# Kernel tuning notes

Measured on AMD Instinct MI355X. Metric: run time of the kernel, lower is better.

The kernel has to match this reference:

```python
import jax, jax.numpy as jnp
import numpy as np

SCALE = 1.0 / np.sqrt(512.0).astype(np.float32)  # attention() hardcodes d_k=512


def setup_inputs() -> dict:
    key = jax.random.key(0)
    ks = jax.random.split(key, 9)
    B, S, D = 4, 2048, 512
    mk = lambda k, shape: jax.random.normal(k, shape, dtype=jnp.float32) * 0.05
    return {
        "q": mk(ks[0], (B, S, D)),
        "k": mk(ks[1], (B, S, D)),
        "v": mk(ks[2], (B, S, D)),
        "WQ_w": mk(ks[3], (D, D)),
        "WQ_b": mk(ks[4], (D,)),
        "WK_w": mk(ks[5], (D, D)),
        "WK_b": mk(ks[6], (D,)),
        "WV_w": mk(ks[7], (D, D)),
        "WV_b": mk(ks[8], (D,)),
    }


def reference(q, k, v, WQ_w, WQ_b, WK_w, WK_b, WV_w, WV_b):
    # torch nn.Linear: y = x @ W.T + b
    qp = q @ WQ_w.T + WQ_b  # [B,S,dk]
    kp = k @ WK_w.T + WK_b  # [B,S,dk]
    vp = v @ WV_w.T + WV_b  # [B,S,dv]
    qk = jnp.einsum("bqd,bkd->bqk", qp, kp) * SCALE  # [B,Sq,Sk]
    S = qk.shape[1]
    tril = jnp.tril(jnp.ones((S, S), dtype=qk.dtype))  # multiplicative causal mask
    qk = qk * tril
    # NOTE: original applies softmax over dim=1 (the query axis), faithfully kept.
    attn = jax.nn.softmax(qk, axis=1)
    out = jnp.einsum("bqk,bkd->bqd", attn, vp)  # [B,Sq,dv]
    return out
```

## Files before the change

### kernel.cpp

```cpp
#include <hip/hip_runtime.h>
#include <hip/hip_bf16.h>


#define S_LEN 2048
#define D_DIM 512
#define SCALE_F 0.044194173824159216f

typedef __attribute__((ext_vector_type(8))) short s8v;
typedef __attribute__((ext_vector_type(4))) short s4v;
typedef __attribute__((ext_vector_type(4))) float f4v;

enum { EPI_BIAS = 0, EPI_BIAS_T = 1, EPI_SCORES = 2 };

#define SBAR()    asm volatile("s_barrier" ::: "memory")
#define WAITV(n)  asm volatile("s_waitcnt vmcnt(" #n ")" ::: "memory")

__device__ __forceinline__ short f2bf_s(float f) {
  union { __hip_bfloat16 b; short s; } u; u.b = __float2bfloat16(f); return u.s;
}
__device__ __forceinline__ float bf2f_s(short h) {
  union { short s; __hip_bfloat16 b; } u; u.s = h; return __bfloat162float(u.b);
}

__device__ __forceinline__ void glds16(const short* g, short* l) {
  __builtin_amdgcn_global_load_lds((const __attribute__((address_space(1))) void*)g,
                                   (__attribute__((address_space(3))) void*)l, 16, 0, 0);
}

template <int EPI>
__device__ __forceinline__ void gemm_core(
    const short* __restrict__ A, const short* __restrict__ B,
    short* __restrict__ C, const float* __restrict__ bias,
    short* SMEM, int N, int K, size_t sCz, int m0, int n0, int bz,
    float* __restrict__ Z)
{
  const int tid  = threadIdx.x;
  const int w    = tid >> 6;
  const int lane = tid & 63;
  const int quad = lane >> 4;
  const int l16  = lane & 15;
  const int wm   = (w >> 1) * 64;
  const int wn   = (w & 1) * 64;

  const int strow = tid >> 2;
  const int gl = ((tid & 3) ^ (strow & 3)) * 8;

  f4v acc[4][4];
#pragma unroll
  for (int i = 0; i < 4; ++i)
#pragma unroll
    for (int j = 0; j < 4; ++j)
#pragma unroll
      for (int r = 0; r < 4; ++r) acc[i][j][r] = 0.0f;

  const short* Ag = A + (size_t)(m0 + strow) * K + gl;
  const short* Bg = B + (size_t)(n0 + strow) * K + gl;
  const size_t pstr = (size_t)64 * K;
  const int t8 = tid * 8;
  const int swq = l16 & 3;

  const int niter = K >> 5;

#pragma unroll
  for (int t = 0; t < 2; ++t) {
    const int k0 = t << 5;
    short* dst = SMEM + t * 8192 + t8;
#pragma unroll
    for (int p = 0; p < 2; ++p) glds16(Ag + k0 + p * pstr, dst + p * 2048);
#pragma unroll
    for (int p = 0; p < 2; ++p) glds16(Bg + k0 + p * pstr, dst + 4096 + p * 2048);
  }

  int cb = 0;
  for (int i = 0; i < niter; ++i) {
    if (i + 1 < niter) { WAITV(4); } else { WAITV(0); }
    SBAR();

    if (i + 2 < niter) {
      int nb = cb + 2; if (nb >= 3) nb -= 3;
      const int k2 = (i + 2) << 5;
      short* dst = SMEM + nb * 8192 + t8;
#pragma unroll
      for (int p = 0; p < 2; ++p) glds16(Ag + k2 + p * pstr, dst + p * 2048);
#pragma unroll
      for (int p = 0; p < 2; ++p) glds16(Bg + k2 + p * pstr, dst + 4096 + p * 2048);
    }

    const short* As = SMEM + cb * 8192;
    const short* Bs = As + 4096;
    cb = (cb == 2) ? 0 : cb + 1;

    s8v af[4], bf[4];
#pragma unroll
    for (int ii = 0; ii < 4; ++ii)
      af[ii] = *(const s8v*)&As[(wm + ii * 16 + l16) * 32 + ((quad ^ swq) * 8)];
#pragma unroll
    for (int j = 0; j < 4; ++j)
      bf[j] = *(const s8v*)&Bs[(wn + j * 16 + l16) * 32 + ((quad ^ swq) * 8)];
#pragma unroll
    for (int ii = 0; ii < 4; ++ii)
#pragma unroll
      for (int j = 0; j < 4; ++j)
        acc[ii][j] = __builtin_amdgcn_mfma_f32_16x16x32_bf16(af[ii], bf[j], acc[ii][j], 0, 0, 0);
  }

  float bv[4];
  if (EPI == EPI_BIAS || EPI == EPI_BIAS_T) {
#pragma unroll
    for (int j = 0; j < 4; ++j) bv[j] = bias[n0 + wn + j * 16 + l16];
  }

  if (EPI == EPI_BIAS_T) {
#pragma unroll
    for (int i = 0; i < 4; ++i) {
#pragma unroll
      for (int j = 0; j < 4; ++j) {
        const int gn  = n0 + wn + j * 16 + l16;
        const int gmb = m0 + wm + i * 16 + quad * 4;
        const int bb = gmb >> 11, ssb = gmb & (S_LEN - 1);
        s4v o;
#pragma unroll
        for (int r = 0; r < 4; ++r) o[r] = f2bf_s(acc[i][j][r] + bv[j]);
        *(s4v*)&C[((size_t)bb * D_DIM + gn) * S_LEN + ssb] = o;
      }
    }
    return;
  }

  short* TB = SMEM;
  const int wbase = w * 2176;
  float csum[4] = {0.f, 0.f, 0.f, 0.f};

#pragma unroll
  for (int ph = 0; ph < 2; ++ph) {
    __syncthreads();
#pragma unroll
    for (int ii = 0; ii < 2; ++ii) {
      const int i = ph * 2 + ii;
#pragma unroll
      for (int j = 0; j < 4; ++j) {
        const int gn = n0 + wn + j * 16 + l16;
#pragma unroll
        for (int r = 0; r < 4; ++r) {
          short o;
          if (EPI == EPI_SCORES) {
            const int gm = m0 + wm + i * 16 + quad * 4 + r;
            const float f = (gm >= gn) ? (__expf(acc[i][j][r] * SCALE_F) - 1.0f) : 0.0f;
            csum[j] += f;
            o = f2bf_s(f);
          } else {
            o = f2bf_s(acc[i][j][r] + bv[j]);
          }
          TB[wbase + (ii * 16 + quad * 4 + r) * 68 + j * 16 + l16] = o;
        }
      }
    }
    __syncthreads();
#pragma unroll
    for (int p = 0; p < 4; ++p) {
      const int row = p * 8 + (lane >> 3);
      const int cg  = lane & 7;
      const s8v vv = *(const s8v*)&TB[wbase + row * 68 + cg * 8];
      const int gm = m0 + wm + ph * 32 + row;
      const int gn = n0 + wn + cg * 8;
      *(s8v*)&C[sCz + (size_t)gm * N + gn] = vv;
    }
  }

  if (EPI == EPI_SCORES) {
#pragma unroll
    for (int j = 0; j < 4; ++j) {
      float cs = csum[j];
      cs += __shfl_xor(cs, 16, 64);
      cs += __shfl_xor(cs, 32, 64);
      if (quad == 0) atomicAdd(&Z[(bz << 11) + n0 + wn + j * 16 + l16], cs);
    }
  }
}

__global__ __launch_bounds__(256, 3) void gemm_scoresF(
    const short* __restrict__ A, const short* __restrict__ B, short* __restrict__ C,
    float* __restrict__ Z)
{
  __shared__ __align__(16) short SMEM[24576];
  const int bz = blockIdx.z;
  const int t = blockIdx.x;
  int ti = (int)((sqrtf(8.0f * t + 1.0f) - 1.0f) * 0.5f);
  while ((ti + 1) * (ti + 2) / 2 <= t) ++ti;
  while (ti * (ti + 1) / 2 > t) --ti;
  const int tj = t - ti * (ti + 1) / 2;
  gemm_core<EPI_SCORES>(A + (size_t)bz * S_LEN * D_DIM, B + (size_t)bz * S_LEN * D_DIM,
                        C, nullptr, SMEM, S_LEN, D_DIM,
                        (size_t)bz * S_LEN * S_LEN, ti * 128, tj * 128, bz, Z);
}

__global__ __launch_bounds__(256, 3) void proj3(
    const short* __restrict__ a0, const short* __restrict__ a1, const short* __restrict__ a2,
    const short* __restrict__ b0, const short* __restrict__ b1, const short* __restrict__ b2,
    short* __restrict__ c0, short* __restrict__ c1, short* __restrict__ c2,
    const float* __restrict__ x0, const float* __restrict__ x1, const float* __restrict__ x2)
{
  __shared__ __align__(16) short SMEM[24576];
  const int z = blockIdx.z;
  const short* A = (z == 0) ? a0 : (z == 1) ? a1 : a2;
  const short* B = (z == 0) ? b0 : (z == 1) ? b1 : b2;
  short*       C = (z == 0) ? c0 : (z == 1) ? c1 : c2;
  const float* bias = (z == 0) ? x0 : (z == 1) ? x1 : x2;
  if (z == 2)
    gemm_core<EPI_BIAS_T>(A, B, C, bias, SMEM, D_DIM, D_DIM, 0,
                          blockIdx.y * 128, blockIdx.x * 128, 0, nullptr);
  else
    gemm_core<EPI_BIAS>(A, B, C, bias, SMEM, D_DIM, D_DIM, 0,
                        blockIdx.y * 128, blockIdx.x * 128, 0, nullptr);
}

__global__ __launch_bounds__(256, 2) void gemm_outF(
    const short* __restrict__ F, const short* __restrict__ vpT,
    const float* __restrict__ Tv, float* __restrict__ out)
{
  __shared__ __align__(16) short SMEM[36864];

  const int tid  = threadIdx.x;
  const int bz   = blockIdx.y;
  const int zs   = blockIdx.z;
  const int mi   = (zs < 16) ? (31 - zs) : (zs - 16);
  const int m0   = mi * 64;
  const int n0   = blockIdx.x * 128;

  const short* A = F   + (size_t)bz * S_LEN * S_LEN;
  const short* B = vpT + (size_t)bz * D_DIM * S_LEN;

  const int w    = tid >> 6;
  const int lane = tid & 63;
  const int quad = lane >> 4;
  const int l16  = lane & 15;
  const int wm   = (w >> 1) * 32;
  const int wn   = (w & 1) * 64;

  const int strow = tid >> 3;
  const int gl = ((tid & 7) ^ (strow & 7)) * 8;

  f4v acc[2][4];
#pragma unroll
  for (int i = 0; i < 2; ++i)
#pragma unroll
    for (int j = 0; j < 4; ++j)
#pragma unroll
      for (int r = 0; r < 4; ++r) acc[i][j][r] = 0.0f;

  const short* Ag = A + (size_t)(m0 + strow) * S_LEN + gl;
  const short* Bg = B + (size_t)(n0 + strow) * S_LEN + gl;
  const size_t pstr = (size_t)32 * S_LEN;
  const int t8 = tid * 8;
  const int swq = l16 & 7;

  const int niter = (m0 >> 6) + 1;

#pragma unroll
  for (int pre = 0; pre < 2; ++pre) {
    short* dst = SMEM + pre * 12288 + t8;
    const int k0 = pre << 6;
#pragma unroll
    for (int p = 0; p < 2; ++p) glds16(Ag + k0 + p * pstr, dst + p * 2048);
#pragma unroll
    for (int p = 0; p < 4; ++p) glds16(Bg + k0 + p * pstr, dst + 4096 + p * 2048);
  }

  int cbuf = 0;
  for (int i = 0; i < niter; ++i) {
    if (i + 1 < niter) { WAITV(6); } else { WAITV(0); }
    SBAR();

    if (i + 2 < niter) {
      int nb = cbuf + 2; if (nb >= 3) nb -= 3;
      const int k2 = (i + 2) << 6;
      short* dst = SMEM + nb * 12288 + t8;
#pragma unroll
      for (int p = 0; p < 2; ++p) glds16(Ag + k2 + p * pstr, dst + p * 2048);
#pragma unroll
      for (int p = 0; p < 4; ++p) glds16(Bg + k2 + p * pstr, dst + 4096 + p * 2048);
    }

    const short* As = SMEM + cbuf * 12288;
    const short* Bs = As + 4096;
    cbuf = (cbuf == 2) ? 0 : cbuf + 1;
#pragma unroll
    for (int kk = 0; kk < 2; ++kk) {
      s8v af[2], bf[4];
#pragma unroll
      for (int ii = 0; ii < 2; ++ii)
        af[ii] = *(const s8v*)&As[(wm + ii * 16 + l16) * 64 + (((kk * 4 + quad) ^ swq) * 8)];
#pragma unroll
      for (int j = 0; j < 4; ++j)
        bf[j] = *(const s8v*)&Bs[(wn + j * 16 + l16) * 64 + (((kk * 4 + quad) ^ swq) * 8)];
#pragma unroll
      for (int ii = 0; ii < 2; ++ii)
#pragma unroll
        for (int j = 0; j < 4; ++j)
          acc[ii][j] = __builtin_amdgcn_mfma_f32_16x16x32_bf16(af[ii], bf[j], acc[ii][j], 0, 0, 0);
    }
  }

  float* Cf = out + (size_t)bz * S_LEN * D_DIM;
#pragma unroll
  for (int i = 0; i < 2; ++i) {
#pragma unroll
    for (int j = 0; j < 4; ++j) {
      const int gn = n0 + wn + j * 16 + l16;
      const float tvn = Tv[(bz << 9) + gn];
#pragma unroll
      for (int r = 0; r < 4; ++r) {
        const int gm = m0 + wm + i * 16 + quad * 4 + r;
        Cf[(size_t)gm * D_DIM + gn] = acc[i][j][r] + tvn;
      }
    }
  }
}

__global__ __launch_bounds__(256) void cvt3(
    const float* __restrict__ s0, const float* __restrict__ s1,
    const float* __restrict__ s2, short* __restrict__ dst, int n)
{
  const float* s = (blockIdx.y == 0) ? s0 : (blockIdx.y == 1) ? s1 : s2;
  short* d = dst + (size_t)blockIdx.y * n;
  const int i = (blockIdx.x * 256 + threadIdx.x) * 8;
  if (i >= n) return;
  const float4 f0 = *(const float4*)(s + i);
  const float4 f1 = *(const float4*)(s + i + 4);
  s8v o;
  o[0] = f2bf_s(f0.x); o[1] = f2bf_s(f0.y); o[2] = f2bf_s(f0.z); o[3] = f2bf_s(f0.w);
  o[4] = f2bf_s(f1.x); o[5] = f2bf_s(f1.y); o[6] = f2bf_s(f1.z); o[7] = f2bf_s(f1.w);
  *(s8v*)(d + i) = o;
}

__global__ __launch_bounds__(256) void scale_vpt_T(
    short* __restrict__ vpT, const float* __restrict__ ZF, float* __restrict__ Tv)
{
  __shared__ float red[4];
  const int b = blockIdx.y, d = blockIdx.x, tid = threadIdx.x;
  const size_t rowbase = ((size_t)(b * D_DIM + d)) * S_LEN;
  const float* zf = ZF + (b << 11);
  const int k0 = tid * 8;

  s8v v = *(s8v*)&vpT[rowbase + k0];
  float s = 0.0f;
#pragma unroll
  for (int i = 0; i < 8; ++i) {
    const float w = bf2f_s(v[i]) / (2048.0f + zf[k0 + i]);
    s += w;
    v[i] = f2bf_s(w);
  }
  *(s8v*)&vpT[rowbase + k0] = v;

#pragma unroll
  for (int off = 32; off >= 1; off >>= 1) s += __shfl_xor(s, off, 64);
  if ((tid & 63) == 0) red[tid >> 6] = s;
  __syncthreads();
  if (tid == 0) Tv[(b << 9) + d] = red[0] + red[1] + red[2] + red[3];
}

extern "C" void kernel_launch(void* const* d_in, const int* in_sizes, int n_in,
                              void* d_out, int out_size, void* d_ws, size_t ws_size,
                              hipStream_t stream) {
  const float* q   = (const float*)d_in[0];
  const float* k   = (const float*)d_in[1];
  const float* v   = (const float*)d_in[2];
  const float* WQw = (const float*)d_in[3];
  const float* WQb = (const float*)d_in[4];
  const float* WKw = (const float*)d_in[5];
  const float* WKb = (const float*)d_in[6];
  const float* WVw = (const float*)d_in[7];
  const float* WVb = (const float*)d_in[8];

  char* ws = (char*)d_ws;
  short* F   = (short*)(ws);
  short* qb  = (short*)(ws);
  short* Wqb = (short*)(ws + 25165824);
  short* qp  = (short*)(ws + 33554432);
  short* kp  = (short*)(ws + 41943040);
  short* vpT = (short*)(ws + 50331648);
  float* ZF  = (float*)(ws + 58720256);
  float* Tv  = (float*)(ws + 58753024);
  short* kb  = qb + 4194304;
  short* vb  = qb + 8388608;
  short* Wkb = Wqb + 262144;
  short* Wvb = Wqb + 524288;

  const dim3 blk(256);

  hipMemsetAsync(ZF, 0, 4 * S_LEN * sizeof(float), stream);

  cvt3<<<dim3(2048, 3), blk, 0, stream>>>(q, k, v, qb, 4194304);
  cvt3<<<dim3(128, 3), blk, 0, stream>>>(WQw, WKw, WVw, Wqb, 262144);

  proj3<<<dim3(4, 64, 3), blk, 0, stream>>>(
      qb, kb, vb, Wqb, Wkb, Wvb, qp, kp, vpT, WQb, WKb, WVb);

  gemm_scoresF<<<dim3(136, 1, 4), blk, 0, stream>>>(qp, kp, F, ZF);

  scale_vpt_T<<<dim3(512, 4), blk, 0, stream>>>(vpT, ZF, Tv);

  gemm_outF<<<dim3(4, 4, 32), blk, 0, stream>>>(F, vpT, Tv, (float*)d_out);
}
```

Baseline: 176.1 us.

## Fuse all stages into one persistent kernel with software grid barriers

```diff
diff --git a/kernel.cpp b/kernel.cpp
--- a/kernel.cpp
+++ b/kernel.cpp
@@ -5,6 +5,7 @@
 #define S_LEN 2048
 #define D_DIM 512
 #define SCALE_F 0.044194173824159216f
+#define NBLK 768
 
 typedef __attribute__((ext_vector_type(8))) short s8v;
 typedef __attribute__((ext_vector_type(4))) short s4v;
@@ -12,8 +13,9 @@
 
 enum { EPI_BIAS = 0, EPI_BIAS_T = 1, EPI_SCORES = 2 };
 
-#define SBAR()    asm volatile("s_barrier" ::: "memory")
-#define WAITV(n)  asm volatile("s_waitcnt vmcnt(" #n ")" ::: "memory")
+#define SBAR()    __builtin_amdgcn_s_barrier()
+#define SCHEDB()  __builtin_amdgcn_sched_barrier(0)
+#define WAITV(n)  asm volatile("s_waitcnt vmcnt(" #n ")")
 
 __device__ __forceinline__ short f2bf_s(float f) {
   union { __hip_bfloat16 b; short s; } u; u.b = __float2bfloat16(f); return u.s;
@@ -25,6 +27,21 @@
 __device__ __forceinline__ void glds16(const short* g, short* l) {
   __builtin_amdgcn_global_load_lds((const __attribute__((address_space(1))) void*)g,
                                    (__attribute__((address_space(3))) void*)l, 16, 0, 0);
+}
+
+__device__ __forceinline__ void gsync(int* bar, int target) {
+  __syncthreads();
+  if (threadIdx.x == 0) {
+    __threadfence();
+    __hip_atomic_fetch_add(bar, 1, __ATOMIC_RELAXED, __HIP_MEMORY_SCOPE_AGENT);
+    int guard = 0;
+    while (__hip_atomic_load(bar, __ATOMIC_RELAXED, __HIP_MEMORY_SCOPE_AGENT) < target) {
+      __builtin_amdgcn_s_sleep(1);
+      if (++guard > (1 << 27)) break;
+    }
+    __threadfence();
+  }
+  __syncthreads();
 }
 
 template <int EPI>
@@ -75,6 +92,7 @@
   for (int i = 0; i < niter; ++i) {
     if (i + 1 < niter) { WAITV(4); } else { WAITV(0); }
     SBAR();
+    SCHEDB();
 
     if (i + 2 < niter) {
       int nb = cb + 2; if (nb >= 3) nb -= 3;
@@ -178,54 +196,14 @@
   }
 }
 
-__global__ __launch_bounds__(256, 3) void gemm_scoresF(
-    const short* __restrict__ A, const short* __restrict__ B, short* __restrict__ C,
-    float* __restrict__ Z)
+__device__ __forceinline__ void outF_body(
+    const short* __restrict__ F, const short* __restrict__ vpT,
+    const float* __restrict__ Tv, float* __restrict__ out,
+    int bz, int zs, int n0, short* SMEM)
 {
-  __shared__ __align__(16) short SMEM[24576];
-  const int bz = blockIdx.z;
-  const int t = blockIdx.x;
-  int ti = (int)((sqrtf(8.0f * t + 1.0f) - 1.0f) * 0.5f);
-  while ((ti + 1) * (ti + 2) / 2 <= t) ++ti;
-  while (ti * (ti + 1) / 2 > t) --ti;
-  const int tj = t - ti * (ti + 1) / 2;
-  gemm_core<EPI_SCORES>(A + (size_t)bz * S_LEN * D_DIM, B + (size_t)bz * S_LEN * D_DIM,
-                        C, nullptr, SMEM, S_LEN, D_DIM,
-                        (size_t)bz * S_LEN * S_LEN, ti * 128, tj * 128, bz, Z);
-}
-
-__global__ __launch_bounds__(256, 3) void proj3(
-    const short* __restrict__ a0, const short* __restrict__ a1, const short* __restrict__ a2,
-    const short* __restrict__ b0, const short* __restrict__ b1, const short* __restrict__ b2,
-    short* __restrict__ c0, short* __restrict__ c1, short* __restrict__ c2,
-    const float* __restrict__ x0, const float* __restrict__ x1, const float* __restrict__ x2)
-{
-  __shared__ __align__(16) short SMEM[24576];
-  const int z = blockIdx.z;
-  const short* A = (z == 0) ? a0 : (z == 1) ? a1 : a2;
-  const short* B = (z == 0) ? b0 : (z == 1) ? b1 : b2;
-  short*       C = (z == 0) ? c0 : (z == 1) ? c1 : c2;
-  const float* bias = (z == 0) ? x0 : (z == 1) ? x1 : x2;
-  if (z == 2)
-    gemm_core<EPI_BIAS_T>(A, B, C, bias, SMEM, D_DIM, D_DIM, 0,
-                          blockIdx.y * 128, blockIdx.x * 128, 0, nullptr);
-  else
-    gemm_core<EPI_BIAS>(A, B, C, bias, SMEM, D_DIM, D_DIM, 0,
-                        blockIdx.y * 128, blockIdx.x * 128, 0, nullptr);
-}
-
-__global__ __launch_bounds__(256, 2) void gemm_outF(
-    const short* __restrict__ F, const short* __restrict__ vpT,
-    const float* __restrict__ Tv, float* __restrict__ out)
-{
-  __shared__ __align__(16) short SMEM[36864];
-
   const int tid  = threadIdx.x;
-  const int bz   = blockIdx.y;
-  const int zs   = blockIdx.z;
   const int mi   = (zs < 16) ? (31 - zs) : (zs - 16);
   const int m0   = mi * 64;
-  const int n0   = blockIdx.x * 128;
 
   const short* A = F   + (size_t)bz * S_LEN * S_LEN;
   const short* B = vpT + (size_t)bz * D_DIM * S_LEN;
@@ -237,8 +215,8 @@
   const int wm   = (w >> 1) * 32;
   const int wn   = (w & 1) * 64;
 
-  const int strow = tid >> 3;
-  const int gl = ((tid & 7) ^ (strow & 7)) * 8;
+  const int strow = tid >> 2;
+  const int gl = ((tid & 3) ^ (strow & 3)) * 8;
 
   f4v acc[2][4];
 #pragma unroll
@@ -250,55 +228,52 @@
 
   const short* Ag = A + (size_t)(m0 + strow) * S_LEN + gl;
   const short* Bg = B + (size_t)(n0 + strow) * S_LEN + gl;
-  const size_t pstr = (size_t)32 * S_LEN;
+  const size_t pstr = (size_t)64 * S_LEN;
   const int t8 = tid * 8;
-  const int swq = l16 & 7;
-
-  const int niter = (m0 >> 6) + 1;
+  const int swq = l16 & 3;
+
+  const int niter = (m0 + 64) >> 5;
 
 #pragma unroll
   for (int pre = 0; pre < 2; ++pre) {
-    short* dst = SMEM + pre * 12288 + t8;
-    const int k0 = pre << 6;
-#pragma unroll
-    for (int p = 0; p < 2; ++p) glds16(Ag + k0 + p * pstr, dst + p * 2048);
-#pragma unroll
-    for (int p = 0; p < 4; ++p) glds16(Bg + k0 + p * pstr, dst + 4096 + p * 2048);
-  }
-
-  int cbuf = 0;
+    short* dst = SMEM + pre * 6144 + t8;
+    const int k0 = pre << 5;
+    glds16(Ag + k0, dst);
+#pragma unroll
+    for (int p = 0; p < 2; ++p) glds16(Bg + k0 + p * pstr, dst + 2048 + p * 2048);
+  }
+
+  int cb = 0;
   for (int i = 0; i < niter; ++i) {
-    if (i + 1 < niter) { WAITV(6); } else { WAITV(0); }
+    if (i + 1 < niter) { WAITV(3); } else { WAITV(0); }
     SBAR();
+    SCHEDB();
 
     if (i + 2 < niter) {
-      int nb = cbuf + 2; if (nb >= 3) nb -= 3;
-      const int k2 = (i + 2) << 6;
-      short* dst = SMEM + nb * 12288 + t8;
-#pragma unroll
-      for (int p = 0; p < 2; ++p) glds16(Ag + k2 + p * pstr, dst + p * 2048);
-#pragma unroll
-      for (int p = 0; p < 4; ++p) glds16(Bg + k2 + p * pstr, dst + 4096 + p * 2048);
-    }
-
-    const short* As = SMEM + cbuf * 12288;
-    const short* Bs = As + 4096;
-    cbuf = (cbuf == 2) ? 0 : cbuf + 1;
-#pragma unroll
-    for (int kk = 0; kk < 2; ++kk) {
-      s8v af[2], bf[4];
-#pragma unroll
-      for (int ii = 0; ii < 2; ++ii)
-        af[ii] = *(const s8v*)&As[(wm + ii * 16 + l16) * 64 + (((kk * 4 + quad) ^ swq) * 8)];
+      int nb = cb + 2; if (nb >= 3) nb -= 3;
+      const int k2 = (i + 2) << 5;
+      short* dst = SMEM + nb * 6144 + t8;
+      glds16(Ag + k2, dst);
+#pragma unroll
+      for (int p = 0; p < 2; ++p) glds16(Bg + k2 + p * pstr, dst + 2048 + p * 2048);
+    }
+
+    const short* As = SMEM + cb * 6144;
+    const short* Bs = As + 2048;
+    cb = (cb == 2) ? 0 : cb + 1;
+
+    s8v af[2], bf[4];
+#pragma unroll
+    for (int ii = 0; ii < 2; ++ii)
+      af[ii] = *(const s8v*)&As[(wm + ii * 16 + l16) * 32 + ((quad ^ swq) * 8)];
+#pragma unroll
+    for (int j = 0; j < 4; ++j)
+      bf[j] = *(const s8v*)&Bs[(wn + j * 16 + l16) * 32 + ((quad ^ swq) * 8)];
+#pragma unroll
+    for (int ii = 0; ii < 2; ++ii)
 #pragma unroll
       for (int j = 0; j < 4; ++j)
-        bf[j] = *(const s8v*)&Bs[(wn + j * 16 + l16) * 64 + (((kk * 4 + quad) ^ swq) * 8)];
-#pragma unroll
-      for (int ii = 0; ii < 2; ++ii)
-#pragma unroll
-        for (int j = 0; j < 4; ++j)
-          acc[ii][j] = __builtin_amdgcn_mfma_f32_16x16x32_bf16(af[ii], bf[j], acc[ii][j], 0, 0, 0);
-    }
+        acc[ii][j] = __builtin_amdgcn_mfma_f32_16x16x32_bf16(af[ii], bf[j], acc[ii][j], 0, 0, 0);
   }
 
   float* Cf = out + (size_t)bz * S_LEN * D_DIM;
@@ -317,46 +292,123 @@
   }
 }
 
-__global__ __launch_bounds__(256) void cvt3(
-    const float* __restrict__ s0, const float* __restrict__ s1,
-    const float* __restrict__ s2, short* __restrict__ dst, int n)
+__global__ __launch_bounds__(256, 3) void fused_all(
+    const float* __restrict__ q, const float* __restrict__ k, const float* __restrict__ v,
+    const float* __restrict__ WQw, const float* __restrict__ WQb,
+    const float* __restrict__ WKw, const float* __restrict__ WKb,
+    const float* __restrict__ WVw, const float* __restrict__ WVb,
+    char* __restrict__ ws, float* __restrict__ out, int* __restrict__ bar)
 {
-  const float* s = (blockIdx.y == 0) ? s0 : (blockIdx.y == 1) ? s1 : s2;
-  short* d = dst + (size_t)blockIdx.y * n;
-  const int i = (blockIdx.x * 256 + threadIdx.x) * 8;
-  if (i >= n) return;
-  const float4 f0 = *(const float4*)(s + i);
-  const float4 f1 = *(const float4*)(s + i + 4);
-  s8v o;
-  o[0] = f2bf_s(f0.x); o[1] = f2bf_s(f0.y); o[2] = f2bf_s(f0.z); o[3] = f2bf_s(f0.w);
-  o[4] = f2bf_s(f1.x); o[5] = f2bf_s(f1.y); o[6] = f2bf_s(f1.z); o[7] = f2bf_s(f1.w);
-  *(s8v*)(d + i) = o;
-}
-
-__global__ __launch_bounds__(256) void scale_vpt_T(
-    short* __restrict__ vpT, const float* __restrict__ ZF, float* __restrict__ Tv)
-{
-  __shared__ float red[4];
-  const int b = blockIdx.y, d = blockIdx.x, tid = threadIdx.x;
-  const size_t rowbase = ((size_t)(b * D_DIM + d)) * S_LEN;
-  const float* zf = ZF + (b << 11);
-  const int k0 = tid * 8;
-
-  s8v v = *(s8v*)&vpT[rowbase + k0];
-  float s = 0.0f;
-#pragma unroll
-  for (int i = 0; i < 8; ++i) {
-    const float w = bf2f_s(v[i]) / (2048.0f + zf[k0 + i]);
-    s += w;
-    v[i] = f2bf_s(w);
-  }
-  *(s8v*)&vpT[rowbase + k0] = v;
-
-#pragma unroll
-  for (int off = 32; off >= 1; off >>= 1) s += __shfl_xor(s, off, 64);
-  if ((tid & 63) == 0) red[tid >> 6] = s;
-  __syncthreads();
-  if (tid == 0) Tv[(b << 9) + d] = red[0] + red[1] + red[2] + red[3];
+  __shared__ __align__(16) short SMEM[24576];
+  __shared__ float red2[4];
+
+  const int bid = blockIdx.x;
+  const int tid = threadIdx.x;
+  const int tg  = bid * 256 + tid;
+
+  short* qb  = (short*)(ws);
+  short* Wqb = (short*)(ws + 25165824);
+  short* qp  = (short*)(ws + 33554432);
+  short* kp  = (short*)(ws + 41943040);
+  short* vpT = (short*)(ws + 50331648);
+  float* ZF  = (float*)(ws + 58720256);
+  float* Tv  = (float*)(ws + 58753024);
+  short* F   = (short*)(ws);
+  short* kb  = qb + 4194304;
+  short* vb  = qb + 8388608;
+  short* Wkb = Wqb + 262144;
+  short* Wvb = Wqb + 524288;
+
+  {
+#pragma unroll 2
+    for (int it = 0; it < 8; ++it) {
+      const int e = (it * 196608 + tg) * 8;
+      const float* s; int off;
+      if (e < 4194304)       { s = q; off = e; }
+      else if (e < 8388608)  { s = k; off = e - 4194304; }
+      else                   { s = v; off = e - 8388608; }
+      const float4 f0 = *(const float4*)(s + off);
+      const float4 f1 = *(const float4*)(s + off + 4);
+      s8v o;
+      o[0] = f2bf_s(f0.x); o[1] = f2bf_s(f0.y); o[2] = f2bf_s(f0.z); o[3] = f2bf_s(f0.w);
+      o[4] = f2bf_s(f1.x); o[5] = f2bf_s(f1.y); o[6] = f2bf_s(f1.z); o[7] = f2bf_s(f1.w);
+      *(s8v*)(qb + e) = o;
+    }
+    if (tg < 98304) {
+      const int e = tg * 8;
+      const float* s; int off;
+      if (e < 262144)        { s = WQw; off = e; }
+      else if (e < 524288)   { s = WKw; off = e - 262144; }
+      else                   { s = WVw; off = e - 524288; }
+      const float4 f0 = *(const float4*)(s + off);
+      const float4 f1 = *(const float4*)(s + off + 4);
+      s8v o;
+      o[0] = f2bf_s(f0.x); o[1] = f2bf_s(f0.y); o[2] = f2bf_s(f0.z); o[3] = f2bf_s(f0.w);
+      o[4] = f2bf_s(f1.x); o[5] = f2bf_s(f1.y); o[6] = f2bf_s(f1.z); o[7] = f2bf_s(f1.w);
+      *(s8v*)((short*)Wqb + e) = o;
+    }
+    if (tg < 8192) ZF[tg] = 0.0f;
+  }
+  gsync(bar, NBLK);
+
+  {
+    const int z   = bid >> 8;
+    const int rem = bid & 255;
+    const int n0  = (rem & 3) * 128;
+    const int m0  = (rem >> 2) * 128;
+    const short* A = (z == 0) ? qb : (z == 1) ? kb : vb;
+    const short* B = (z == 0) ? Wqb : (z == 1) ? Wkb : Wvb;
+    short*       C = (z == 0) ? qp : (z == 1) ? kp : vpT;
+    const float* bias = (z == 0) ? WQb : (z == 1) ? WKb : WVb;
+    if (z == 2)
+      gemm_core<EPI_BIAS_T>(A, B, C, bias, SMEM, D_DIM, D_DIM, 0, m0, n0, 0, nullptr);
+    else
+      gemm_core<EPI_BIAS>(A, B, C, bias, SMEM, D_DIM, D_DIM, 0, m0, n0, 0, nullptr);
+  }
+  gsync(bar, 2 * NBLK);
+
+  if (bid < 544) {
+    const int bz = bid / 136;
+    const int t  = bid - bz * 136;
+    int ti = (int)((sqrtf(8.0f * t + 1.0f) - 1.0f) * 0.5f);
+    while ((ti + 1) * (ti + 2) / 2 <= t) ++ti;
+    while (ti * (ti + 1) / 2 > t) --ti;
+    const int tj = t - ti * (ti + 1) / 2;
+    gemm_core<EPI_SCORES>(qp + (size_t)bz * S_LEN * D_DIM, kp + (size_t)bz * S_LEN * D_DIM,
+                          F, nullptr, SMEM, S_LEN, D_DIM,
+                          (size_t)bz * S_LEN * S_LEN, ti * 128, tj * 128, bz, ZF);
+  }
+  gsync(bar, 3 * NBLK);
+
+  for (int r = bid; r < 2048; r += NBLK) {
+    __syncthreads();
+    const int b = r >> 9, d = r & 511;
+    const size_t rowbase = ((size_t)(b * D_DIM + d)) * S_LEN;
+    const float* zf = ZF + (b << 11);
+    const int k0 = tid * 8;
+    s8v vv = *(s8v*)&vpT[rowbase + k0];
+    float s = 0.0f;
+#pragma unroll
+    for (int i = 0; i < 8; ++i) {
+      const float wgt = bf2f_s(vv[i]) / (2048.0f + zf[k0 + i]);
+      s += wgt;
+      vv[i] = f2bf_s(wgt);
+    }
+    *(s8v*)&vpT[rowbase + k0] = vv;
+#pragma unroll
+    for (int off = 32; off >= 1; off >>= 1) s += __shfl_xor(s, off, 64);
+    if ((tid & 63) == 0) red2[tid >> 6] = s;
+    __syncthreads();
+    if (tid == 0) Tv[(b << 9) + d] = red2[0] + red2[1] + red2[2] + red2[3];
+  }
+  gsync(bar, 4 * NBLK);
+
+  if (bid < 512) {
+    const int n0 = (bid & 3) * 128;
+    const int bz = (bid >> 2) & 3;
+    const int zs = bid >> 4;
+    outF_body(F, vpT, Tv, out, bz, zs, n0, SMEM);
+  }
 }
 
 extern "C" void kernel_launch(void* const* d_in, const int* in_sizes, int n_in,
@@ -372,33 +424,10 @@
   const float* WVw = (const float*)d_in[7];
   const float* WVb = (const float*)d_in[8];
 
-  char* ws = (char*)d_ws;
-  short* F   = (short*)(ws);
-  short* qb  = (short*)(ws);
-  short* Wqb = (short*)(ws + 25165824);
-  short* qp  = (short*)(ws + 33554432);
-  short* kp  = (short*)(ws + 41943040);
-  short* vpT = (short*)(ws + 50331648);
-  float* ZF  = (float*)(ws + 58720256);
-  float* Tv  = (float*)(ws + 58753024);
-  short* kb  = qb + 4194304;
-  short* vb  = qb + 8388608;
-  short* Wkb = Wqb + 262144;
-  short* Wvb = Wqb + 524288;
-
-  const dim3 blk(256);
-
-  hipMemsetAsync(ZF, 0, 4 * S_LEN * sizeof(float), stream);
-
-  cvt3<<<dim3(2048, 3), blk, 0, stream>>>(q, k, v, qb, 4194304);
-  cvt3<<<dim3(128, 3), blk, 0, stream>>>(WQw, WKw, WVw, Wqb, 262144);
-
-  proj3<<<dim3(4, 64, 3), blk, 0, stream>>>(
-      qb, kb, vb, Wqb, Wkb, Wvb, qp, kp, vpT, WQb, WKb, WVb);
-
-  gemm_scoresF<<<dim3(136, 1, 4), blk, 0, stream>>>(qp, kp, F, ZF);
-
-  scale_vpt_T<<<dim3(512, 4), blk, 0, stream>>>(vpT, ZF, Tv);
-
-  gemm_outF<<<dim3(4, 4, 32), blk, 0, stream>>>(F, vpT, Tv, (float*)d_out);
-}
+  int* bar = (int*)d_out;
+  hipMemsetAsync(bar, 0, 64, stream);
+
+  fused_all<<<dim3(NBLK), dim3(256), 0, stream>>>(
+      q, k, v, WQw, WQb, WKw, WKb, WVw, WVb,
+      (char*)d_ws, (float*)d_out, bar);
+}
```

Result: slower. 542.4 us (+208.0%).
